# Optimization experiments

Hardware: AMD Instinct MI355X
Metric: run time of the kernel (lower is better)

## Reference

```python
import jax, jax.numpy as jnp
import numpy as np

C = 256
C8 = C // 8
B, D, H, W = 1, 8, 32, 32
N = D * H * W


def setup_inputs() -> dict:
    key = jax.random.key(0)
    ks = jax.random.split(key, 16)
    s = 0.02
    inp = {
        'x': jax.random.normal(ks[0], (B, C, D, H, W), dtype=jnp.float32),
        'WqA': jax.random.normal(ks[1], (C8, C), dtype=jnp.float32) * s,
        'bqA': jnp.zeros((C8,), dtype=jnp.float32),
        'WkA': jax.random.normal(ks[2], (C8, C), dtype=jnp.float32) * s,
        'bkA': jnp.zeros((C8,), dtype=jnp.float32),
        'WvA': jax.random.normal(ks[3], (C, C), dtype=jnp.float32) * s,
        'bvA': jnp.zeros((C,), dtype=jnp.float32),
        'WqB': jax.random.normal(ks[4], (C8, C), dtype=jnp.float32) * s,
        'bqB': jnp.zeros((C8,), dtype=jnp.float32),
        'WkB': jax.random.normal(ks[5], (C8, C), dtype=jnp.float32) * s,
        'bkB': jnp.zeros((C8,), dtype=jnp.float32),
        'WvB': jax.random.normal(ks[6], (C, C), dtype=jnp.float32) * s,
        'bvB': jnp.zeros((C,), dtype=jnp.float32),
        'gamma_A': jax.random.normal(ks[7], (1,), dtype=jnp.float32) * 0.5,
        'gamma_B': jax.random.normal(ks[8], (1,), dtype=jnp.float32) * 0.5,
    }
    return inp


def _conv1x1(Wt, b, xf):
    # 1x1x1 Conv3d on flattened volume: [Cout,Cin] x [B,Cin,N] -> [B,Cout,N]
    return jnp.einsum('oc,bcn->bon', Wt, xf) + b[None, :, None]


def reference(x, WqA, bqA, WkA, bkA, WvA, bvA, WqB, bqB, WkB, bkB, WvB, bvB, gamma_A, gamma_B):
    b_, c_, d_, h_, w_ = x.shape
    n = d_ * h_ * w_
    xf = x.reshape(b_, c_, n)  # [B,C,N]

    QA = _conv1x1(WqA, bqA, xf)  # [B,C8,N]
    KA = _conv1x1(WkA, bkA, xf)
    VA = _conv1x1(WvA, bvA, xf)  # [B,C,N]
    QB = _conv1x1(WqB, bqB, xf)
    KB = _conv1x1(WkB, bkB, xf)
    VB = _conv1x1(WvB, bvB, xf)

    # attention_B_A[b,n,m] = softmax_m( QB^T KA )
    attn_BA = jax.nn.softmax(jnp.einsum('bcn,bcm->bnm', QB, KA), axis=-1)
    # F_B_new = V_A @ attn_BA^T
    F_B = jnp.einsum('bcm,bnm->bcn', VA, attn_BA).reshape(b_, c_, d_, h_, w_)

    attn_AB = jax.nn.softmax(jnp.einsum('bcn,bcm->bnm', QA, KB), axis=-1)
    F_A = jnp.einsum('bcm,bnm->bcn', VB, attn_AB).reshape(b_, c_, d_, h_, w_)

    out_task1 = gamma_A[0] * F_A + x
    out_task2 = gamma_B[0] * F_B + x
    return (out_task1, out_task2)
```

## Files before the change

### kernel.cpp

```cpp
#include <hip/hip_runtime.h>

#define N 8192
#define CIN 256
#define C8 32
#define QBLK 128
#define KVB 64

typedef __attribute__((ext_vector_type(8))) short short8;
typedef __attribute__((ext_vector_type(4))) float f32x4;
typedef __attribute__((ext_vector_type(2))) float f32x2;
typedef __attribute__((ext_vector_type(4))) float float4_;
typedef __attribute__((ext_vector_type(4))) unsigned uint4_;
typedef __attribute__((ext_vector_type(2))) unsigned uint2_;

#define OFF_QTA 0u
#define OFF_KTA 262144u
#define OFF_QTB 524288u
#define OFF_KTB 786432u
#define OFF_VA  1048576u
#define OFF_VB  3145728u
#define PROJ_USHORTS 5242880u

__device__ __forceinline__ unsigned short f2bf(float f) {
    unsigned u = __builtin_bit_cast(unsigned, f);
    u += 0x7fffu + ((u >> 16) & 1u);
    return (unsigned short)(u >> 16);
}
__device__ __forceinline__ unsigned packbf2(float a, float b) {
    return (unsigned)f2bf(a) | ((unsigned)f2bf(b) << 16);
}
__device__ __forceinline__ float bf2f(unsigned short u) {
    return __builtin_bit_cast(float, (unsigned)u << 16);
}

__device__ __forceinline__ int swz_off(int row, int mu) {
    return (row << 7) + (((mu ^ (row & 7)) & 7) << 4);
}

__global__ __launch_bounds__(256) void proj_kernel(
    const float* __restrict__ x,
    const float* __restrict__ WqA, const float* __restrict__ bqA,
    const float* __restrict__ WkA, const float* __restrict__ bkA,
    const float* __restrict__ WvA, const float* __restrict__ bvA,
    const float* __restrict__ WqB, const float* __restrict__ bqB,
    const float* __restrict__ WkB, const float* __restrict__ bkB,
    const float* __restrict__ WvB, const float* __restrict__ bvB,
    unsigned short* __restrict__ ws)
{
    __shared__ __align__(16) float Wlds[16 * 256];

    const int t = threadIdx.x;
    const int n = blockIdx.x * 256 + t;
    const int rg = blockIdx.y;

    const float* W; const float* bias; unsigned short* dst; int orel; int trans;
    if (rg < 2)       { W = WqA; bias = bqA; dst = ws + OFF_QTA; orel = rg * 16;        trans = 1; }
    else if (rg < 4)  { W = WkA; bias = bkA; dst = ws + OFF_KTA; orel = (rg - 2) * 16;  trans = 1; }
    else if (rg < 20) { W = WvA; bias = bvA; dst = ws + OFF_VA;  orel = (rg - 4) * 16;  trans = 0; }
    else if (rg < 22) { W = WqB; bias = bqB; dst = ws + OFF_QTB; orel = (rg - 20) * 16; trans = 1; }
    else if (rg < 24) { W = WkB; bias = bkB; dst = ws + OFF_KTB; orel = (rg - 22) * 16; trans = 1; }
    else              { W = WvB; bias = bvB; dst = ws + OFF_VB;  orel = (rg - 24) * 16; trans = 0; }

    {
        const float4_* Wg = (const float4_*)(W + (size_t)orel * CIN);
        float4_* Wl = (float4_*)Wlds;
        #pragma unroll
        for (int b = 0; b < 4; ++b) Wl[b * 256 + t] = Wg[b * 256 + t];
    }
    __syncthreads();

    f32x2 acc2[16];
    #pragma unroll
    for (int o = 0; o < 16; ++o) acc2[o] = (f32x2){0.f, 0.f};

    const f32x2* W2 = (const f32x2*)Wlds;
    for (int c0 = 0; c0 < CIN; c0 += 8) {
        f32x2 xv[4];
        #pragma unroll
        for (int k = 0; k < 4; ++k) {
            xv[k].x = x[(size_t)(c0 + 2 * k) * N + n];
            xv[k].y = x[(size_t)(c0 + 2 * k + 1) * N + n];
        }
        #pragma unroll
        for (int o = 0; o < 16; ++o) {
            const f32x2* wr = W2 + o * 128 + (c0 >> 1);
            #pragma unroll
            for (int k = 0; k < 4; ++k) acc2[o] += wr[k] * xv[k];
        }
    }

    float acc[16];
    #pragma unroll
    for (int o = 0; o < 16; ++o) acc[o] = acc2[o].x + acc2[o].y + bias[orel + o];

    if (trans) {
        unsigned pk[8];
        #pragma unroll
        for (int q = 0; q < 8; ++q) pk[q] = packbf2(acc[2*q], acc[2*q+1]);
        unsigned* p = (unsigned*)(dst + (size_t)n * 32 + orel);
        *(uint4_*)(p)     = (uint4_){pk[0], pk[1], pk[2], pk[3]};
        *(uint4_*)(p + 4) = (uint4_){pk[4], pk[5], pk[6], pk[7]};
    } else {
        #pragma unroll
        for (int o = 0; o < 16; ++o) dst[(size_t)(orel + o) * N + n] = f2bf(acc[o]);
    }
}

__global__ __launch_bounds__(512, 2) void attn_kernel(
    const unsigned short* __restrict__ ws,
    unsigned short* __restrict__ accb,
    float* __restrict__ Lpart,
    int SP)
{
    __shared__ __align__(16) unsigned short Vt[256 * 64];
    __shared__ __align__(16) unsigned short Pl[128 * 64];

    const int tid = threadIdx.x;
    const int w = tid >> 6, l = tid & 63, g = l >> 4, lc = l & 15;
    const int bid = blockIdx.x;
    const int dir = bid & 1;
    const int qb  = (bid >> 1) & 63;
    const int sp  = bid >> 7;
    const int mlen   = N / SP;
    const int m_base = sp * mlen;
    const int NS     = mlen / KVB;

    const unsigned short* qt = ws + (dir ? OFF_QTA : OFF_QTB);
    const unsigned short* kt = ws + (dir ? OFF_KTB : OFF_KTA);
    const unsigned short* V  = ws + (dir ? OFF_VB  : OFF_VA);

    const float L2E = 1.4426950408889634f;

    const short8 qf = *(const short8*)(qt + (size_t)(qb * QBLK + w * 16 + lc) * C8 + 8 * g);

    #pragma unroll
    for (int h = 0; h < 4; ++h) {
        const int c = ((w * 4 + h) << 3) + (l >> 3);
        const int slot = l & 7;
        const unsigned short* src = V + (size_t)c * N + m_base + (((slot ^ (c & 7)) & 7) << 3);
        unsigned short* dstl = Vt + ((w * 4 + h) << 9);
        __builtin_amdgcn_global_load_lds((const __attribute__((address_space(1))) unsigned int*)src,
                                         (__attribute__((address_space(3))) unsigned int*)dstl,
                                         16, 0, 0);
    }
    short8 kf[4], kfn[4];
    #pragma unroll
    for (int t = 0; t < 4; ++t)
        kf[t] = *(const short8*)(kt + (size_t)(m_base + 16 * t + lc) * C8 + 8 * g);

    f32x4 acc[2][8];
    #pragma unroll
    for (int u = 0; u < 2; ++u)
        #pragma unroll
        for (int j = 0; j < 8; ++j) acc[u][j] = (f32x4){0.f, 0.f, 0.f, 0.f};
    float Lr = 0.f;

    const int col = w * 16 + lc;

    for (int s = 0; s < NS; ++s) {
        const int m0 = m_base + s * KVB;

        f32x4 sv[4];
        #pragma unroll
        for (int t = 0; t < 4; ++t)
            sv[t] = __builtin_amdgcn_mfma_f32_16x16x32_bf16(kf[t], qf, (f32x4){0.f,0.f,0.f,0.f}, 0, 0, 0);

        float pr[4][4];
        #pragma unroll
        for (int t = 0; t < 4; ++t)
            #pragma unroll
            for (int i = 0; i < 4; ++i) {
                pr[t][i] = exp2f(fminf(sv[t][i] * L2E, 80.f));
                Lr += pr[t][i];
            }
        #pragma unroll
        for (int t = 0; t < 4; ++t) {
            uint2_ u2;
            u2.x = packbf2(pr[t][0], pr[t][1]);
            u2.y = packbf2(pr[t][2], pr[t][3]);
            *(uint2_*)((char*)Pl + swz_off(col, 2 * t + (g >> 1)) + ((g & 1) << 3)) = u2;
        }

        __syncthreads();

        if (s + 1 < NS) {
            #pragma unroll
            for (int t = 0; t < 4; ++t)
                kfn[t] = *(const short8*)(kt + (size_t)(m0 + KVB + 16 * t + lc) * C8 + 8 * g);
        }

        short8 vf[2][2];
        #pragma unroll
        for (int u = 0; u < 2; ++u)
            #pragma unroll
            for (int kc = 0; kc < 2; ++kc)
                vf[u][kc] = *(const short8*)((const char*)Vt + swz_off(w * 32 + u * 16 + lc, kc * 4 + g));

        #pragma unroll
        for (int j = 0; j < 8; ++j) {
            const int colr = j * 16 + lc;
            const short8 pf0 = *(const short8*)((const char*)Pl + swz_off(colr, g));
            const short8 pf1 = *(const short8*)((const char*)Pl + swz_off(colr, 4 + g));
            #pragma unroll
            for (int u = 0; u < 2; ++u) {
                acc[u][j] = __builtin_amdgcn_mfma_f32_16x16x32_bf16(vf[u][0], pf0, acc[u][j], 0, 0, 0);
                acc[u][j] = __builtin_amdgcn_mfma_f32_16x16x32_bf16(vf[u][1], pf1, acc[u][j], 0, 0, 0);
            }
        }

        __syncthreads();

        if (s + 1 < NS) {
            #pragma unroll
            for (int h = 0; h < 4; ++h) {
                const int c = ((w * 4 + h) << 3) + (l >> 3);
                const int slot = l & 7;
                const unsigned short* src = V + (size_t)c * N + (m0 + KVB) + (((slot ^ (c & 7)) & 7) << 3);
                unsigned short* dstl = Vt + ((w * 4 + h) << 9);
                __builtin_amdgcn_global_load_lds((const __attribute__((address_space(1))) unsigned int*)src,
                                                 (__attribute__((address_space(3))) unsigned int*)dstl,
                                                 16, 0, 0);
            }
            #pragma unroll
            for (int t = 0; t < 4; ++t) kf[t] = kfn[t];
        }
    }

    Lr += __shfl_xor(Lr, 16);
    Lr += __shfl_xor(Lr, 32);
    __syncthreads();
    float* Lsh = (float*)Pl;
    if (g == 0) Lsh[w * 16 + lc] = Lr;
    __syncthreads();

    const size_t blk = (size_t)(dir * 64 + qb) * SP + sp;
    unsigned short* ab = accb + blk * (256 * 128);
    #pragma unroll
    for (int u = 0; u < 2; ++u)
        #pragma unroll
        for (int j = 0; j < 8; ++j)
            #pragma unroll
            for (int i = 0; i < 4; ++i) {
                const int c  = w * 32 + u * 16 + 4 * g + i;
                const int nl = j * 16 + lc;
                ab[c * 128 + nl] = f2bf(acc[u][j][i]);
            }
    if (tid < 128) Lpart[blk * 128 + tid] = Lsh[tid];
}

__global__ __launch_bounds__(256) void combine_kernel(
    const float* __restrict__ x,
    const unsigned short* __restrict__ accb,
    const float* __restrict__ Lpart,
    const float* __restrict__ gammaA, const float* __restrict__ gammaB,
    float* __restrict__ out, int SP)
{
    const int tid = blockIdx.x * 256 + threadIdx.x;
    const int nlq = tid & 15;
    const int qb  = (tid >> 4) & 63;
    const int c   = (tid >> 10) & 255;
    const int dir = (tid >> 18) & 1;
    const int nl0 = nlq * 8;

    const size_t bb = (size_t)(dir * 64 + qb) * SP;
    float s[8], Ls[8];
    #pragma unroll
    for (int e = 0; e < 8; ++e) { s[e] = 0.f; Ls[e] = 0.f; }

    for (int sp = 0; sp < SP; ++sp) {
        const unsigned short* ap = accb + (bb + sp) * (256 * 128) + (size_t)c * 128 + nl0;
        const short8 av = *(const short8*)ap;
        const float* lp = Lpart + (bb + sp) * 128 + nl0;
        #pragma unroll
        for (int e = 0; e < 8; ++e) {
            s[e]  += bf2f((unsigned short)av[e]);
            Ls[e] += lp[e];
        }
    }

    const float gamma = dir ? gammaA[0] : gammaB[0];
    const size_t off = (size_t)c * N + qb * QBLK + nl0;
    const float* xp = x + off;
    float* op = out + (dir ? 0 : (size_t)CIN * N) + off;
    #pragma unroll
    for (int e = 0; e < 8; ++e) op[e] = gamma * s[e] / Ls[e] + xp[e];
}

extern "C" void kernel_launch(void* const* d_in, const int* in_sizes, int n_in,
                              void* d_out, int out_size, void* d_ws, size_t ws_size,
                              hipStream_t stream) {
    const float* x = (const float*)d_in[0];
    unsigned short* ws = (unsigned short*)d_ws;

    size_t needed4 = (size_t)PROJ_USHORTS * 2 + 4ull * 8388608 + 4ull * 65536;
    size_t needed2 = (size_t)PROJ_USHORTS * 2 + 2ull * 8388608 + 2ull * 65536;
    int SP = (ws_size >= needed4) ? 4 : (ws_size >= needed2) ? 2 : 1;

    unsigned short* accb = ws + PROJ_USHORTS;
    float* Lpart = (float*)(ws + PROJ_USHORTS + (size_t)SP * 4194304);

    dim3 pg(32, 40);
    proj_kernel<<<pg, 256, 0, stream>>>(
        x,
        (const float*)d_in[1],  (const float*)d_in[2],
        (const float*)d_in[3],  (const float*)d_in[4],
        (const float*)d_in[5],  (const float*)d_in[6],
        (const float*)d_in[7],  (const float*)d_in[8],
        (const float*)d_in[9],  (const float*)d_in[10],
        (const float*)d_in[11], (const float*)d_in[12],
        ws);

    attn_kernel<<<128 * SP, 512, 0, stream>>>(ws, accb, Lpart, SP);

    combine_kernel<<<2048, 256, 0, stream>>>(
        x, accb, Lpart,
        (const float*)d_in[13], (const float*)d_in[14],
        (float*)d_out, SP);
}
```

Baseline: 273.5 us.

## Move projections to bf16 MFMA, halve query block, double-buffer V and P in attention

Adds a kernel that casts the weights to bf16, folding the log2(e) factor into the Q weights and Q bias. The projection kernel becomes an MFMA GEMM over an LDS-transposed, swizzled bf16 tile of x. Attention now uses 64-query blocks with twice as many workgroups and a higher occupancy bound. V and P tiles are double-buffered so the next V stage loads during compute, dropping one barrier per step, and the exponent uses raw exp2 with no clamp. Only four of the eight waves compute scores, and the exp2 overflow clamp is gone, so very large logits could now overflow.

Measured after the change: 224.9 us. -17.8%, faster.

```diff
diff --git a/kernel.cpp b/kernel.cpp
--- a/kernel.cpp
+++ b/kernel.cpp
@@ -3,14 +3,14 @@
 #define N 8192
 #define CIN 256
 #define C8 32
-#define QBLK 128
+#define QBLK 64
 #define KVB 64
+#define L2E 1.4426950408889634f
 
 typedef __attribute__((ext_vector_type(8))) short short8;
 typedef __attribute__((ext_vector_type(4))) float f32x4;
-typedef __attribute__((ext_vector_type(2))) float f32x2;
 typedef __attribute__((ext_vector_type(4))) float float4_;
-typedef __attribute__((ext_vector_type(4))) unsigned uint4_;
+typedef __attribute__((ext_vector_type(4))) unsigned short ushort4_;
 typedef __attribute__((ext_vector_type(2))) unsigned uint2_;
 
 #define OFF_QTA 0u
@@ -33,94 +33,125 @@
     return __builtin_bit_cast(float, (unsigned)u << 16);
 }
 
-__device__ __forceinline__ int swz_off(int row, int mu) {
-    return (row << 7) + (((mu ^ (row & 7)) & 7) << 4);
-}
-
-__global__ __launch_bounds__(256) void proj_kernel(
-    const float* __restrict__ x,
-    const float* __restrict__ WqA, const float* __restrict__ bqA,
-    const float* __restrict__ WkA, const float* __restrict__ bkA,
-    const float* __restrict__ WvA, const float* __restrict__ bvA,
-    const float* __restrict__ WqB, const float* __restrict__ bqB,
-    const float* __restrict__ WkB, const float* __restrict__ bkB,
-    const float* __restrict__ WvB, const float* __restrict__ bvB,
+__global__ __launch_bounds__(256) void castw_kernel(
+    const float* __restrict__ WqA, const float* __restrict__ WkA, const float* __restrict__ WvA,
+    const float* __restrict__ WqB, const float* __restrict__ WkB, const float* __restrict__ WvB,
+    unsigned short* __restrict__ Wb)
+{
+    const int idx = blockIdx.x * 256 + threadIdx.x;
+    const int e = idx * 4;
+    const int r = e >> 8;
+    const float* src; int rel;
+    if (r < 32)       { src = WqA; rel = e; }
+    else if (r < 64)  { src = WkA; rel = e - 32 * 256; }
+    else if (r < 320) { src = WvA; rel = e - 64 * 256; }
+    else if (r < 352) { src = WqB; rel = e - 320 * 256; }
+    else if (r < 384) { src = WkB; rel = e - 352 * 256; }
+    else              { src = WvB; rel = e - 384 * 256; }
+    const float sc = (r < 32 || (r >= 320 && r < 352)) ? L2E : 1.0f;
+    float4_ v = *(const float4_*)(src + rel);
+    ushort4_ o;
+    o.x = f2bf(v.x * sc); o.y = f2bf(v.y * sc); o.z = f2bf(v.z * sc); o.w = f2bf(v.w * sc);
+    *(ushort4_*)(Wb + e) = o;
+}
+
+__global__ __launch_bounds__(512) void proj_kernel(
+    const float* __restrict__ x, const unsigned short* __restrict__ Wb,
+    const float* __restrict__ bqA, const float* __restrict__ bkA, const float* __restrict__ bvA,
+    const float* __restrict__ bqB, const float* __restrict__ bkB, const float* __restrict__ bvB,
     unsigned short* __restrict__ ws)
 {
-    __shared__ __align__(16) float Wlds[16 * 256];
-
-    const int t = threadIdx.x;
-    const int n = blockIdx.x * 256 + t;
-    const int rg = blockIdx.y;
-
-    const float* W; const float* bias; unsigned short* dst; int orel; int trans;
-    if (rg < 2)       { W = WqA; bias = bqA; dst = ws + OFF_QTA; orel = rg * 16;        trans = 1; }
-    else if (rg < 4)  { W = WkA; bias = bkA; dst = ws + OFF_KTA; orel = (rg - 2) * 16;  trans = 1; }
-    else if (rg < 20) { W = WvA; bias = bvA; dst = ws + OFF_VA;  orel = (rg - 4) * 16;  trans = 0; }
-    else if (rg < 22) { W = WqB; bias = bqB; dst = ws + OFF_QTB; orel = (rg - 20) * 16; trans = 1; }
-    else if (rg < 24) { W = WkB; bias = bkB; dst = ws + OFF_KTB; orel = (rg - 22) * 16; trans = 1; }
-    else              { W = WvB; bias = bvB; dst = ws + OFF_VB;  orel = (rg - 24) * 16; trans = 0; }
-
-    {
-        const float4_* Wg = (const float4_*)(W + (size_t)orel * CIN);
-        float4_* Wl = (float4_*)Wlds;
-        #pragma unroll
-        for (int b = 0; b < 4; ++b) Wl[b * 256 + t] = Wg[b * 256 + t];
+    __shared__ __align__(16) unsigned short xT[32 * 256];
+
+    const int tid = threadIdx.x;
+    const int w = tid >> 6, l = tid & 63, g = l >> 4, lc = l & 15;
+    const int n0 = blockIdx.x * 32;
+
+    #pragma unroll
+    for (int r = 0; r < 4; ++r) {
+        const int flat4 = r * 512 + tid;
+        const int c = flat4 >> 3, nl = (flat4 & 7) * 4;
+        float4_ v = *(const float4_*)(x + (size_t)c * N + n0 + nl);
+        #pragma unroll
+        for (int e = 0; e < 4; ++e) {
+            const int nn = nl + e;
+            const int byte = nn * 512 + ((2 * c) ^ ((nn & 7) << 4));
+            *(unsigned short*)((char*)xT + byte) = f2bf(v[e]);
+        }
     }
     __syncthreads();
 
-    f32x2 acc2[16];
-    #pragma unroll
-    for (int o = 0; o < 16; ++o) acc2[o] = (f32x2){0.f, 0.f};
-
-    const f32x2* W2 = (const f32x2*)Wlds;
-    for (int c0 = 0; c0 < CIN; c0 += 8) {
-        f32x2 xv[4];
-        #pragma unroll
-        for (int k = 0; k < 4; ++k) {
-            xv[k].x = x[(size_t)(c0 + 2 * k) * N + n];
-            xv[k].y = x[(size_t)(c0 + 2 * k + 1) * N + n];
-        }
-        #pragma unroll
-        for (int o = 0; o < 16; ++o) {
-            const f32x2* wr = W2 + o * 128 + (c0 >> 1);
-            #pragma unroll
-            for (int k = 0; k < 4; ++k) acc2[o] += wr[k] * xv[k];
-        }
-    }
-
-    float acc[16];
-    #pragma unroll
-    for (int o = 0; o < 16; ++o) acc[o] = acc2[o].x + acc2[o].y + bias[orel + o];
-
-    if (trans) {
-        unsigned pk[8];
-        #pragma unroll
-        for (int q = 0; q < 8; ++q) pk[q] = packbf2(acc[2*q], acc[2*q+1]);
-        unsigned* p = (unsigned*)(dst + (size_t)n * 32 + orel);
-        *(uint4_*)(p)     = (uint4_){pk[0], pk[1], pk[2], pk[3]};
-        *(uint4_*)(p + 4) = (uint4_){pk[4], pk[5], pk[6], pk[7]};
-    } else {
-        #pragma unroll
-        for (int o = 0; o < 16; ++o) dst[(size_t)(orel + o) * N + n] = f2bf(acc[o]);
-    }
-}
-
-__global__ __launch_bounds__(512, 2) void attn_kernel(
+    f32x4 acc[5][2];
+    #pragma unroll
+    for (int i = 0; i < 5; ++i)
+        #pragma unroll
+        for (int ns = 0; ns < 2; ++ns) acc[i][ns] = (f32x4){0.f, 0.f, 0.f, 0.f};
+
+    for (int c0 = 0; c0 < 256; c0 += 32) {
+        short8 xf[2];
+        #pragma unroll
+        for (int ns = 0; ns < 2; ++ns) {
+            const int byte = (ns * 16 + lc) * 512 + ((2 * (c0 + 8 * g)) ^ ((lc & 7) << 4));
+            xf[ns] = *(const short8*)((const char*)xT + byte);
+        }
+        #pragma unroll
+        for (int i = 0; i < 5; ++i) {
+            const int ot = w * 5 + i;
+            const short8 wf = *(const short8*)(Wb + (size_t)(ot * 16 + lc) * 256 + c0 + 8 * g);
+            const bool isV = (ot >= 4 && ot < 20) || (ot >= 24);
+            #pragma unroll
+            for (int ns = 0; ns < 2; ++ns)
+                acc[i][ns] = isV
+                    ? __builtin_amdgcn_mfma_f32_16x16x32_bf16(wf, xf[ns], acc[i][ns], 0, 0, 0)
+                    : __builtin_amdgcn_mfma_f32_16x16x32_bf16(xf[ns], wf, acc[i][ns], 0, 0, 0);
+        }
+    }
+
+    #pragma unroll
+    for (int i = 0; i < 5; ++i) {
+        const int ot = w * 5 + i;
+        const float* bias; unsigned short* dst; int orelm; bool isV = false; float bsc = 1.0f;
+        if (ot < 2)       { bias = bqA; dst = ws + OFF_QTA; orelm = ot * 16;        bsc = L2E; }
+        else if (ot < 4)  { bias = bkA; dst = ws + OFF_KTA; orelm = (ot - 2) * 16; }
+        else if (ot < 20) { bias = bvA; dst = ws + OFF_VA;  orelm = (ot - 4) * 16;  isV = true; }
+        else if (ot < 22) { bias = bqB; dst = ws + OFF_QTB; orelm = (ot - 20) * 16; bsc = L2E; }
+        else if (ot < 24) { bias = bkB; dst = ws + OFF_KTB; orelm = (ot - 22) * 16; }
+        else              { bias = bvB; dst = ws + OFF_VB;  orelm = (ot - 24) * 16; isV = true; }
+
+        if (isV) {
+            #pragma unroll
+            for (int ii = 0; ii < 4; ++ii) {
+                const float b = bias[orelm + 4 * g + ii];
+                #pragma unroll
+                for (int ns = 0; ns < 2; ++ns)
+                    dst[(size_t)(orelm + 4 * g + ii) * N + n0 + ns * 16 + lc] = f2bf(acc[i][ns][ii] + b);
+            }
+        } else {
+            const float b = bias[orelm + lc] * bsc;
+            #pragma unroll
+            for (int ns = 0; ns < 2; ++ns)
+                #pragma unroll
+                for (int ii = 0; ii < 4; ++ii)
+                    dst[(size_t)(n0 + ns * 16 + 4 * g + ii) * C8 + orelm + lc] = f2bf(acc[i][ns][ii] + b);
+        }
+    }
+}
+
+__global__ __launch_bounds__(512, 4) void attn_kernel(
     const unsigned short* __restrict__ ws,
     unsigned short* __restrict__ accb,
     float* __restrict__ Lpart,
     int SP)
 {
-    __shared__ __align__(16) unsigned short Vt[256 * 64];
-    __shared__ __align__(16) unsigned short Pl[128 * 64];
+    __shared__ __align__(16) unsigned short Vt[2][256 * 64];
+    __shared__ __align__(16) unsigned short Pl[2][64 * 64];
 
     const int tid = threadIdx.x;
     const int w = tid >> 6, l = tid & 63, g = l >> 4, lc = l & 15;
     const int bid = blockIdx.x;
     const int dir = bid & 1;
-    const int qb  = (bid >> 1) & 63;
-    const int sp  = bid >> 7;
+    const int qb  = (bid >> 1) & 127;
+    const int sp  = bid >> 8;
     const int mlen   = N / SP;
     const int m_base = sp * mlen;
     const int NS     = mlen / KVB;
@@ -129,123 +160,123 @@
     const unsigned short* kt = ws + (dir ? OFF_KTB : OFF_KTA);
     const unsigned short* V  = ws + (dir ? OFF_VB  : OFF_VA);
 
-    const float L2E = 1.4426950408889634f;
-
-    const short8 qf = *(const short8*)(qt + (size_t)(qb * QBLK + w * 16 + lc) * C8 + 8 * g);
-
-    #pragma unroll
-    for (int h = 0; h < 4; ++h) {
-        const int c = ((w * 4 + h) << 3) + (l >> 3);
-        const int slot = l & 7;
-        const unsigned short* src = V + (size_t)c * N + m_base + (((slot ^ (c & 7)) & 7) << 3);
-        unsigned short* dstl = Vt + ((w * 4 + h) << 9);
-        __builtin_amdgcn_global_load_lds((const __attribute__((address_space(1))) unsigned int*)src,
-                                         (__attribute__((address_space(3))) unsigned int*)dstl,
-                                         16, 0, 0);
-    }
+    const bool sw = (w < 4);
+    const int col = w * 16 + lc;
+
+    short8 qf = {};
+    if (sw) qf = *(const short8*)(qt + (size_t)(qb * QBLK + col) * C8 + 8 * g);
+
+    const int src_c   = w * 32 + (l >> 3);
+    const int src_swz = ((l & 7) ^ ((l >> 3) & 7)) << 3;
+    #define STAGE(vb, mo)                                                                 \
+        _Pragma("unroll")                                                                 \
+        for (int h = 0; h < 4; ++h) {                                                     \
+            const unsigned short* srcp = V + (size_t)(src_c + 8 * h) * N + (mo) + src_swz; \
+            __builtin_amdgcn_global_load_lds(                                             \
+                (const __attribute__((address_space(1))) unsigned*)srcp,                  \
+                (__attribute__((address_space(3))) unsigned*)(&Vt[vb][(w * 32 + h * 8) * 64]), \
+                16, 0, 0);                                                                \
+        }
+
+    STAGE(0, m_base)
+
     short8 kf[4], kfn[4];
-    #pragma unroll
-    for (int t = 0; t < 4; ++t)
-        kf[t] = *(const short8*)(kt + (size_t)(m_base + 16 * t + lc) * C8 + 8 * g);
-
-    f32x4 acc[2][8];
+    if (sw) {
+        #pragma unroll
+        for (int t = 0; t < 4; ++t)
+            kf[t] = *(const short8*)(kt + (size_t)(m_base + 16 * t + lc) * C8 + 8 * g);
+    }
+
+    f32x4 acc[2][4];
     #pragma unroll
     for (int u = 0; u < 2; ++u)
         #pragma unroll
-        for (int j = 0; j < 8; ++j) acc[u][j] = (f32x4){0.f, 0.f, 0.f, 0.f};
+        for (int j = 0; j < 4; ++j) acc[u][j] = (f32x4){0.f, 0.f, 0.f, 0.f};
     float Lr = 0.f;
-
-    const int col = w * 16 + lc;
 
     for (int s = 0; s < NS; ++s) {
         const int m0 = m_base + s * KVB;
-
-        f32x4 sv[4];
-        #pragma unroll
-        for (int t = 0; t < 4; ++t)
-            sv[t] = __builtin_amdgcn_mfma_f32_16x16x32_bf16(kf[t], qf, (f32x4){0.f,0.f,0.f,0.f}, 0, 0, 0);
-
-        float pr[4][4];
-        #pragma unroll
-        for (int t = 0; t < 4; ++t)
-            #pragma unroll
-            for (int i = 0; i < 4; ++i) {
-                pr[t][i] = exp2f(fminf(sv[t][i] * L2E, 80.f));
-                Lr += pr[t][i];
+        const int pb = s & 1;
+
+        if (sw) {
+            if (s + 1 < NS) {
+                #pragma unroll
+                for (int t = 0; t < 4; ++t)
+                    kfn[t] = *(const short8*)(kt + (size_t)(m0 + KVB + 16 * t + lc) * C8 + 8 * g);
             }
-        #pragma unroll
-        for (int t = 0; t < 4; ++t) {
-            uint2_ u2;
-            u2.x = packbf2(pr[t][0], pr[t][1]);
-            u2.y = packbf2(pr[t][2], pr[t][3]);
-            *(uint2_*)((char*)Pl + swz_off(col, 2 * t + (g >> 1)) + ((g & 1) << 3)) = u2;
+            f32x4 sv[4];
+            #pragma unroll
+            for (int t = 0; t < 4; ++t)
+                sv[t] = __builtin_amdgcn_mfma_f32_16x16x32_bf16(kf[t], qf, (f32x4){0.f,0.f,0.f,0.f}, 0, 0, 0);
+
+            float pr[4][4];
+            #pragma unroll
+            for (int t = 0; t < 4; ++t)
+                #pragma unroll
+                for (int i = 0; i < 4; ++i) {
+                    pr[t][i] = __builtin_amdgcn_exp2f(sv[t][i]);
+                    Lr += pr[t][i];
+                }
+            #pragma unroll
+            for (int t = 0; t < 4; ++t) {
+                uint2_ u2;
+                u2.x = packbf2(pr[t][0], pr[t][1]);
+                u2.y = packbf2(pr[t][2], pr[t][3]);
+                const int byte = col * 128 + ((((2 * t + (g >> 1)) ^ (col & 7)) << 4)) + ((g & 1) << 3);
+                *(uint2_*)((char*)Pl[pb] + byte) = u2;
+            }
         }
 
         __syncthreads();
 
-        if (s + 1 < NS) {
-            #pragma unroll
-            for (int t = 0; t < 4; ++t)
-                kfn[t] = *(const short8*)(kt + (size_t)(m0 + KVB + 16 * t + lc) * C8 + 8 * g);
-        }
-
+        if (s + 1 < NS) STAGE(pb ^ 1, m0 + KVB)
+
+        __builtin_amdgcn_s_setprio(1);
         short8 vf[2][2];
         #pragma unroll
         for (int u = 0; u < 2; ++u)
             #pragma unroll
             for (int kc = 0; kc < 2; ++kc)
-                vf[u][kc] = *(const short8*)((const char*)Vt + swz_off(w * 32 + u * 16 + lc, kc * 4 + g));
-
-        #pragma unroll
-        for (int j = 0; j < 8; ++j) {
-            const int colr = j * 16 + lc;
-            const short8 pf0 = *(const short8*)((const char*)Pl + swz_off(colr, g));
-            const short8 pf1 = *(const short8*)((const char*)Pl + swz_off(colr, 4 + g));
-            #pragma unroll
-            for (int u = 0; u < 2; ++u) {
-                acc[u][j] = __builtin_amdgcn_mfma_f32_16x16x32_bf16(vf[u][0], pf0, acc[u][j], 0, 0, 0);
-                acc[u][j] = __builtin_amdgcn_mfma_f32_16x16x32_bf16(vf[u][1], pf1, acc[u][j], 0, 0, 0);
-            }
-        }
-
-        __syncthreads();
-
-        if (s + 1 < NS) {
-            #pragma unroll
-            for (int h = 0; h < 4; ++h) {
-                const int c = ((w * 4 + h) << 3) + (l >> 3);
-                const int slot = l & 7;
-                const unsigned short* src = V + (size_t)c * N + (m0 + KVB) + (((slot ^ (c & 7)) & 7) << 3);
-                unsigned short* dstl = Vt + ((w * 4 + h) << 9);
-                __builtin_amdgcn_global_load_lds((const __attribute__((address_space(1))) unsigned int*)src,
-                                                 (__attribute__((address_space(3))) unsigned int*)dstl,
-                                                 16, 0, 0);
-            }
+                vf[u][kc] = *(const short8*)((const char*)Vt[pb]
+                              + (w * 32 + u * 16 + lc) * 128 + (((kc * 4 + g) ^ (lc & 7)) << 4));
+        #pragma unroll
+        for (int kc = 0; kc < 2; ++kc) {
+            short8 pf[4];
+            #pragma unroll
+            for (int j = 0; j < 4; ++j)
+                pf[j] = *(const short8*)((const char*)Pl[pb]
+                          + (j * 16 + lc) * 128 + (((kc * 4 + g) ^ (lc & 7)) << 4));
+            #pragma unroll
+            for (int u = 0; u < 2; ++u)
+                #pragma unroll
+                for (int j = 0; j < 4; ++j)
+                    acc[u][j] = __builtin_amdgcn_mfma_f32_16x16x32_bf16(vf[u][kc], pf[j], acc[u][j], 0, 0, 0);
+        }
+        __builtin_amdgcn_s_setprio(0);
+
+        if (sw && s + 1 < NS) {
             #pragma unroll
             for (int t = 0; t < 4; ++t) kf[t] = kfn[t];
         }
     }
 
-    Lr += __shfl_xor(Lr, 16);
-    Lr += __shfl_xor(Lr, 32);
-    __syncthreads();
-    float* Lsh = (float*)Pl;
-    if (g == 0) Lsh[w * 16 + lc] = Lr;
-    __syncthreads();
-
-    const size_t blk = (size_t)(dir * 64 + qb) * SP + sp;
-    unsigned short* ab = accb + blk * (256 * 128);
+    if (sw) {
+        Lr += __shfl_xor(Lr, 16);
+        Lr += __shfl_xor(Lr, 32);
+    }
+    const size_t blk = (size_t)(dir * 128 + qb) * SP + sp;
+    unsigned short* ab = accb + blk * (256 * 64);
     #pragma unroll
     for (int u = 0; u < 2; ++u)
         #pragma unroll
-        for (int j = 0; j < 8; ++j)
+        for (int j = 0; j < 4; ++j)
             #pragma unroll
             for (int i = 0; i < 4; ++i) {
                 const int c  = w * 32 + u * 16 + 4 * g + i;
                 const int nl = j * 16 + lc;
-                ab[c * 128 + nl] = f2bf(acc[u][j][i]);
+                ab[c * 64 + nl] = f2bf(acc[u][j][i]);
             }
-    if (tid < 128) Lpart[blk * 128 + tid] = Lsh[tid];
+    if (sw && l < 16) Lpart[blk * 64 + w * 16 + l] = Lr;
 }
 
 __global__ __launch_bounds__(256) void combine_kernel(
@@ -256,21 +287,20 @@
     float* __restrict__ out, int SP)
 {
     const int tid = blockIdx.x * 256 + threadIdx.x;
-    const int nlq = tid & 15;
-    const int qb  = (tid >> 4) & 63;
+    const int nl0 = (tid & 7) * 8;
+    const int qb  = (tid >> 3) & 127;
     const int c   = (tid >> 10) & 255;
     const int dir = (tid >> 18) & 1;
-    const int nl0 = nlq * 8;
-
-    const size_t bb = (size_t)(dir * 64 + qb) * SP;
+
+    const size_t bb = (size_t)(dir * 128 + qb) * SP;
     float s[8], Ls[8];
     #pragma unroll
     for (int e = 0; e < 8; ++e) { s[e] = 0.f; Ls[e] = 0.f; }
 
     for (int sp = 0; sp < SP; ++sp) {
-        const unsigned short* ap = accb + (bb + sp) * (256 * 128) + (size_t)c * 128 + nl0;
+        const unsigned short* ap = accb + (bb + sp) * (256 * 64) + (size_t)c * 64 + nl0;
         const short8 av = *(const short8*)ap;
-        const float* lp = Lpart + (bb + sp) * 128 + nl0;
+        const float* lp = Lpart + (bb + sp) * 64 + nl0;
         #pragma unroll
         for (int e = 0; e < 8; ++e) {
             s[e]  += bf2f((unsigned short)av[e]);
@@ -297,20 +327,20 @@
     int SP = (ws_size >= needed4) ? 4 : (ws_size >= needed2) ? 2 : 1;
 
     unsigned short* accb = ws + PROJ_USHORTS;
+    unsigned short* Wb   = accb;
     float* Lpart = (float*)(ws + PROJ_USHORTS + (size_t)SP * 4194304);
 
-    dim3 pg(32, 40);
-    proj_kernel<<<pg, 256, 0, stream>>>(
-        x,
-        (const float*)d_in[1],  (const float*)d_in[2],
-        (const float*)d_in[3],  (const float*)d_in[4],
-        (const float*)d_in[5],  (const float*)d_in[6],
-        (const float*)d_in[7],  (const float*)d_in[8],
-        (const float*)d_in[9],  (const float*)d_in[10],
-        (const float*)d_in[11], (const float*)d_in[12],
+    castw_kernel<<<160, 256, 0, stream>>>(
+        (const float*)d_in[1], (const float*)d_in[3], (const float*)d_in[5],
+        (const float*)d_in[7], (const float*)d_in[9], (const float*)d_in[11], Wb);
+
+    proj_kernel<<<256, 512, 0, stream>>>(
+        x, Wb,
+        (const float*)d_in[2],  (const float*)d_in[4],  (const float*)d_in[6],
+        (const float*)d_in[8],  (const float*)d_in[10], (const float*)d_in[12],
         ws);
 
-    attn_kernel<<<128 * SP, 512, 0, stream>>>(ws, accb, Lpart, SP);
+    attn_kernel<<<256 * SP, 512, 0, stream>>>(ws, accb, Lpart, SP);
 
     combine_kernel<<<2048, 256, 0, stream>>>(
         x, accb, Lpart,
```
